# Optimization experiments

Hardware: AMD Instinct MI355X
Metric: run time of the kernel (lower is better)

Reference implementation:

```python
import jax, jax.numpy as jnp
import numpy as np

NUM_HEADS = 8
LN_EPS = 1e-5


def setup_inputs() -> dict:
    key = jax.random.key(0)
    ks = jax.random.split(key, 8)
    B, H, W, C = 2, 64, 64, 256
    return {
        "x": jax.random.normal(ks[0], (B, H, W, C), dtype=jnp.float32),
        "cond": jax.random.normal(ks[1], (B, C), dtype=jnp.float32),
        "t": jax.random.randint(ks[2], (B,), 0, 100, dtype=jnp.int64),
        "emb_table": jax.random.normal(ks[3], (100, C), dtype=jnp.float32) * 0.02,
        "ada_w": jax.random.normal(ks[4], (C, 2 * C), dtype=jnp.float32) * 0.02,
        "ada_b": jnp.zeros((2 * C,), dtype=jnp.float32),
        "qkv_w": jax.random.normal(ks[5], (C, 3 * C), dtype=jnp.float32) * 0.02,
        "qkv_b": jnp.zeros((3 * C,), dtype=jnp.float32),
        "proj_w": jax.random.normal(ks[6], (C, C), dtype=jnp.float32) * 0.02,
        "proj_b": jnp.zeros((C,), dtype=jnp.float32),
    }


def reference(x, cond, t, emb_table, ada_w, ada_b, qkv_w, qkv_b, proj_w, proj_b):
    B, H, W, C = x.shape
    N = H * W
    h = NUM_HEADS
    d = C // h
    scale = d ** -0.5

    x = x.reshape(B, N, C)

    # AdaLayerNorm (adalayernorm_abs): timestep embedding -> SiLU -> Linear -> scale/shift
    emb = emb_table[t]                                # [B, C]
    ss = jax.nn.silu(emb) @ ada_w + ada_b             # [B, 2C]
    sc, sh = jnp.split(ss, 2, axis=-1)                # each [B, C]
    mu = jnp.mean(x, axis=-1, keepdims=True)
    var = jnp.var(x, axis=-1, keepdims=True)
    xn = (x - mu) * jax.lax.rsqrt(var + LN_EPS)       # LN without affine
    x = xn * (1.0 + sc[:, None, :]) + sh[:, None, :]

    # QKV projection and head split
    qkv = (x @ qkv_w + qkv_b).reshape(B, N, 3, h, d)
    qkv = jnp.transpose(qkv, (2, 0, 3, 1, 4))          # [3, B, h, N, d]
    q, k, v = qkv[0], qkv[1], qkv[2]

    # Manual attention: full [B, h, N, N] scores (matches original module)
    attn = jnp.einsum('bhnd,bhmd->bhnm', q, k) * scale
    attn = jax.nn.softmax(attn, axis=-1)
    out = jnp.einsum('bhnm,bhmd->bhnd', attn, v)       # [B, h, N, d]
    out = jnp.transpose(out, (0, 2, 1, 3)).reshape(B, N, C)

    out = (out.reshape(B, H, W, C) @ proj_w) + proj_b
    return out
```

## Files before the change

kernel.cpp:

```cpp
#include <hip/hip_runtime.h>
#include <hip/hip_bf16.h>
#include <stdint.h>

typedef __attribute__((ext_vector_type(8))) short bfrag;
typedef __attribute__((ext_vector_type(4))) short bfrag4;
typedef __attribute__((ext_vector_type(4))) float f32x4;
typedef __attribute__((ext_vector_type(2))) float f32x2;
typedef __attribute__((ext_vector_type(2))) unsigned int u32x2;

__device__ inline short f2bf(float f) {
  union { float f; uint32_t u; } v; v.f = f;
  uint32_t u = v.u;
  uint32_t r = (u + 0x7fffu + ((u >> 16) & 1u)) >> 16;
  return (short)r;
}
__device__ inline float bf2f(short s) {
  return __builtin_bit_cast(float, (uint32_t)((uint32_t)(uint16_t)s << 16));
}

#if __has_builtin(__builtin_amdgcn_cvt_pk_bf16_f32)
typedef __attribute__((ext_vector_type(2))) __bf16 bf16x2_t;
__device__ inline uint32_t pack_bf16(float a, float b) {
  bf16x2_t r = __builtin_amdgcn_cvt_pk_bf16_f32(a, b);
  return __builtin_bit_cast(uint32_t, r);
}
#else
__device__ inline uint32_t pack_bf16(float a, float b) {
  uint32_t ua = __builtin_bit_cast(uint32_t, a) + 0x8000u;
  uint32_t ub = __builtin_bit_cast(uint32_t, b) + 0x8000u;
  return __builtin_amdgcn_perm(ub, ua, 0x07060302);
}
#endif

__global__ __launch_bounds__(256) void prep_kernel(
    const float* __restrict__ emb_table, const int* __restrict__ t,
    const float* __restrict__ ada_w, const float* __restrict__ ada_b,
    float* __restrict__ scsh,
    const float* __restrict__ qkv_w, short* __restrict__ qkv_wt,
    const float* __restrict__ proj_w, short* __restrict__ proj_wt) {
  __shared__ float smem[64 * 65];
  const int blk = blockIdx.x;
  const int tid = threadIdx.x;
  if (blk < 16) {
    float* se = smem;
    float* part = smem + 256;
    int b = blk >> 3, ox = blk & 7;
    int tt = t[b];
    float e = emb_table[tt * 256 + tid];
    se[tid] = e / (1.f + __expf(-e));
    __syncthreads();
    int ol = tid & 63, kc = tid >> 6;
    int o = ox * 64 + ol;
    float acc = 0.f;
#pragma unroll 8
    for (int k = kc * 64; k < (kc + 1) * 64; ++k) acc += se[k] * ada_w[k * 512 + o];
    part[tid] = acc;
    __syncthreads();
    if (tid < 64) {
      int oo = ox * 64 + tid;
      scsh[b * 512 + oo] =
          part[tid] + part[64 + tid] + part[128 + tid] + part[192 + tid] + ada_b[oo];
    }
  } else {
    const float* W; short* Wt; int N, lb;
    if (blk < 64) { W = qkv_w; Wt = qkv_wt; N = 768; lb = blk - 16; }
    else          { W = proj_w; Wt = proj_wt; N = 256; lb = blk - 64; }
    float (*tile)[65] = (float(*)[65])smem;
    int k0 = (lb & 3) * 64, n0 = (lb >> 2) * 64;
    int r = tid >> 2, c0 = (tid & 3) * 16;
    const float* src = W + (long)(k0 + r) * N + n0 + c0;
#pragma unroll
    for (int j = 0; j < 16; j += 4) {
      float4 v = *(const float4*)(src + j);
      tile[r][c0 + j] = v.x; tile[r][c0 + j + 1] = v.y;
      tile[r][c0 + j + 2] = v.z; tile[r][c0 + j + 3] = v.w;
    }
    __syncthreads();
    int nl = tid >> 2, kc = (tid & 3) * 16;
    short outv[16];
#pragma unroll
    for (int j = 0; j < 16; ++j) outv[j] = f2bf(tile[kc + j][nl]);
    short* dst = Wt + (long)(n0 + nl) * 256 + k0 + kc;
    *(bfrag*)dst = *(bfrag*)&outv[0];
    *(bfrag*)(dst + 8) = *(bfrag*)&outv[8];
  }
}

__global__ __launch_bounds__(256) void ln_kernel(const float* __restrict__ x,
                                                 const float* __restrict__ scsh,
                                                 short* __restrict__ xb) {
  int row = blockIdx.x * 4 + (threadIdx.x >> 6);
  int b = row >> 12;
  int lane = threadIdx.x & 63;
  float4 v = *(const float4*)(x + (long)row * 256 + lane * 4);
  float s = v.x + v.y + v.z + v.w;
  float sq = v.x * v.x + v.y * v.y + v.z * v.z + v.w * v.w;
#pragma unroll
  for (int off = 32; off > 0; off >>= 1) {
    s += __shfl_xor(s, off);
    sq += __shfl_xor(sq, off);
  }
  float mu = s * (1.f / 256.f);
  float var = sq * (1.f / 256.f) - mu * mu;
  float rstd = rsqrtf(var + 1e-5f);
  const float* scp = scsh + b * 512 + lane * 4;
  float4 sc = *(const float4*)scp;
  float4 sh = *(const float4*)(scp + 256);
  float y0 = (v.x - mu) * rstd * (1.f + sc.x) + sh.x;
  float y1 = (v.y - mu) * rstd * (1.f + sc.y) + sh.y;
  float y2 = (v.z - mu) * rstd * (1.f + sc.z) + sh.z;
  float y3 = (v.w - mu) * rstd * (1.f + sc.w) + sh.w;
  u32x2 o; o.x = pack_bf16(y0, y1); o.y = pack_bf16(y2, y3);
  *(u32x2*)&xb[(long)row * 256 + lane * 4] = o;
}

__global__ __launch_bounds__(256) void gemm_qkv(const short* __restrict__ A,
                                                const short* __restrict__ Bt,
                                                const float* __restrict__ bias,
                                                float qscale,
                                                short* __restrict__ qk,
                                                short* __restrict__ vT) {
  __shared__ short As[128 * 40];
  __shared__ short Bs[64 * 40];
  const int mt = blockIdx.x, nt = blockIdx.y;
  const int tid = threadIdx.x;
  const int w = tid >> 6, lane = tid & 63, l16 = lane & 15, quad = lane >> 4;
  const int ar = tid >> 1, ak = (tid & 1) * 16;
  const int br = tid >> 2, bk = (tid & 3) * 8;
  f32x4 acc[2][4] = {};
  const short* Arow = A + (long)(mt * 128 + ar) * 256 + ak;
  const short* Brow = Bt + (long)(nt * 64 + br) * 256 + bk;
  bfrag a8a = *(const bfrag*)Arow;
  bfrag a8b = *(const bfrag*)(Arow + 8);
  bfrag b8  = *(const bfrag*)Brow;
  for (int kk = 0; kk < 8; ++kk) {
    __syncthreads();
    *(bfrag*)&As[ar * 40 + ak] = a8a;
    *(bfrag*)&As[ar * 40 + ak + 8] = a8b;
    *(bfrag*)&Bs[br * 40 + bk] = b8;
    __syncthreads();
    int kn = (kk < 7) ? (kk + 1) : 7;
    a8a = *(const bfrag*)(Arow + kn * 32);
    a8b = *(const bfrag*)(Arow + kn * 32 + 8);
    b8  = *(const bfrag*)(Brow + kn * 32);
    bfrag a0 = *(const bfrag*)&As[(w * 32 + l16) * 40 + quad * 8];
    bfrag a1 = *(const bfrag*)&As[(w * 32 + 16 + l16) * 40 + quad * 8];
#pragma unroll
    for (int c = 0; c < 4; ++c) {
      bfrag bf = *(const bfrag*)&Bs[(c * 16 + l16) * 40 + quad * 8];
      acc[0][c] = __builtin_amdgcn_mfma_f32_16x16x32_bf16(a0, bf, acc[0][c], 0, 0, 0);
      acc[1][c] = __builtin_amdgcn_mfma_f32_16x16x32_bf16(a1, bf, acc[1][c], 0, 0, 0);
    }
  }
  const int rowb = mt * 128 + w * 32 + quad * 4;
  if (nt < 8) {
#pragma unroll
    for (int rg = 0; rg < 2; ++rg) {
      int row0 = rowb + rg * 16;
#pragma unroll
      for (int c = 0; c < 4; ++c) {
        int col = nt * 64 + c * 16 + l16;
        float bv = bias[col];
        float mult = (col < 256) ? qscale : 1.0f;
#pragma unroll
        for (int r = 0; r < 4; ++r)
          qk[(long)(row0 + r) * 512 + col] = f2bf((acc[rg][c][r] + bv) * mult);
      }
    }
  } else {
    const int bb = mt >> 5;
#pragma unroll
    for (int rg = 0; rg < 2; ++rg) {
      int keyl = (rowb + rg * 16) & 4095;
#pragma unroll
      for (int c = 0; c < 4; ++c) {
        int col = nt * 64 + c * 16 + l16;
        float bv = bias[col];
        int d = col - 512;
        u32x2 dd;
        dd.x = pack_bf16(acc[rg][c][0] + bv, acc[rg][c][1] + bv);
        dd.y = pack_bf16(acc[rg][c][2] + bv, acc[rg][c][3] + bv);
        *(u32x2*)&vT[((long)(bb * 8 + (d >> 5)) * 32 + (d & 31)) * 4096 + keyl] = dd;
      }
    }
  }
}

__global__ __launch_bounds__(256) void attn_kernel(const short* __restrict__ qk,
                                                   const short* __restrict__ vT,
                                                   short* __restrict__ OpB,
                                                   float* __restrict__ lpart) {
  const int blk = blockIdx.x;
  const int qt = blk & 15;
  const int bh = (blk >> 4) & 15;
  const int ks = blk >> 8;
  const int b = bh >> 3, hh = bh & 7;
  const int tid = threadIdx.x;
  const int w = tid >> 6, lane = tid & 63, l16 = lane & 15, quad = lane >> 4;

  __shared__ short Ks[2][64 * 40];
  __shared__ short Vt[2][32 * 68];

  const long rowbase = (long)b * 4096;
  const int qrow0 = qt * 256 + w * 64 + l16;
  bfrag qf[4];
#pragma unroll
  for (int g = 0; g < 4; ++g)
    qf[g] = *(const bfrag*)&qk[(rowbase + qrow0 + g * 16) * 512 + hh * 32 + quad * 8];

  f32x4 o0[4] = {}, o1[4] = {};
  f32x2 lsum[4] = {};

  const int si = tid >> 2, sk = (tid & 3) * 8;
  const int vrow = tid >> 3, vcol = (tid & 7) * 8;
  const short* ksrc = qk + rowbase * 512 + 256 + hh * 32 + (long)si * 512 + sk;
  const short* vsrc = vT + ((long)bh * 32 + vrow) * 4096 + vcol;

  const int kt0 = ks * 16;
  bfrag k8 = *(const bfrag*)(ksrc + (long)kt0 * 64 * 512);
  bfrag v8 = *(const bfrag*)(vsrc + kt0 * 64);

  int buf = 0;
  for (int i = 0; i < 16; ++i) {
    *(bfrag*)&Ks[buf][si * 40 + sk] = k8;
    *(bfrag*)&Vt[buf][vrow * 68 + vcol] = v8;
    __syncthreads();
    int nn = (i < 15) ? (i + 1) : 15;
    k8 = *(const bfrag*)(ksrc + (long)(kt0 + nn) * 64 * 512);
    v8 = *(const bfrag*)(vsrc + (kt0 + nn) * 64);

#pragma unroll
    for (int nt = 0; nt < 4; ++nt) {
      bfrag kf = *(const bfrag*)&Ks[buf][(nt * 16 + l16) * 40 + quad * 8];
      f32x4 z = {0,0,0,0};
      f32x4 s[4];
      s[0] = __builtin_amdgcn_mfma_f32_16x16x32_bf16(kf, qf[0], z, 0, 0, 0);
      s[1] = __builtin_amdgcn_mfma_f32_16x16x32_bf16(kf, qf[1], z, 0, 0, 0);
      s[2] = __builtin_amdgcn_mfma_f32_16x16x32_bf16(kf, qf[2], z, 0, 0, 0);
      s[3] = __builtin_amdgcn_mfma_f32_16x16x32_bf16(kf, qf[3], z, 0, 0, 0);
      bfrag4 pb[4];
#pragma unroll
      for (int g = 0; g < 4; ++g) {
        float p0 = __builtin_amdgcn_exp2f(s[g][0]);
        float p1 = __builtin_amdgcn_exp2f(s[g][1]);
        float p2 = __builtin_amdgcn_exp2f(s[g][2]);
        float p3 = __builtin_amdgcn_exp2f(s[g][3]);
        f32x2 pa = {p0, p1}, pc = {p2, p3};
        lsum[g] += pa; lsum[g] += pc;
        u32x2 pk; pk.x = pack_bf16(p0, p1); pk.y = pack_bf16(p2, p3);
        pb[g] = __builtin_bit_cast(bfrag4, pk);
      }
      bfrag4 va = *(const bfrag4*)&Vt[buf][l16 * 68 + nt * 16 + quad * 4];
      bfrag4 vb = *(const bfrag4*)&Vt[buf][(16 + l16) * 68 + nt * 16 + quad * 4];
#pragma unroll
      for (int g = 0; g < 4; ++g) {
        o0[g] = __builtin_amdgcn_mfma_f32_16x16x16bf16_1k(va, pb[g], o0[g], 0, 0, 0);
        o1[g] = __builtin_amdgcn_mfma_f32_16x16x16bf16_1k(vb, pb[g], o1[g], 0, 0, 0);
      }
    }
    buf ^= 1;
  }
#pragma unroll
  for (int g = 0; g < 4; ++g) {
    float ls = lsum[g].x + lsum[g].y;
    ls += __shfl_xor(ls, 16); ls += __shfl_xor(ls, 32);
    const long pbase = (((long)ks * 16 + bh) * 4096 + qrow0 + g * 16) * 32;
    u32x2 dA, dB;
    dA.x = pack_bf16(o0[g][0], o0[g][1]); dA.y = pack_bf16(o0[g][2], o0[g][3]);
    dB.x = pack_bf16(o1[g][0], o1[g][1]); dB.y = pack_bf16(o1[g][2], o1[g][3]);
    *(u32x2*)&OpB[pbase + quad * 4] = dA;
    *(u32x2*)&OpB[pbase + 16 + quad * 4] = dB;
    if (quad == 0)
      lpart[((long)ks * 16 + bh) * 4096 + qrow0 + g * 16] = ls;
  }
}

__global__ __launch_bounds__(256) void proj_kernel(const short* __restrict__ OpB,
                                                   const float* __restrict__ lpart,
                                                   const short* __restrict__ Bt,
                                                   const float* __restrict__ bias,
                                                   float* __restrict__ out) {
  __shared__ short As[128 * 40];
  __shared__ short Bs[64 * 40];
  const int mt = blockIdx.x, nt = blockIdx.y;
  const int tid = threadIdx.x;
  const int w = tid >> 6, lane = tid & 63, l16 = lane & 15, quad = lane >> 4;
  const int ar = tid >> 1, ak = (tid & 1) * 16;
  const int br = tid >> 2, bk = (tid & 3) * 8;
  f32x4 acc[2][4] = {};

  const int row = mt * 128 + ar;
  const int q = row & 4095, bq = row >> 12;
  const short* Brow = Bt + (long)(nt * 64 + br) * 256 + bk;

  long lb0 = (long)(bq * 8) * 4096 + q;
  bfrag pa[4][2];
  f32x4 pl;
#pragma unroll
  for (int ks = 0; ks < 4; ++ks) {
    long base = (lb0 + (long)ks * 16 * 4096) * 32 + ak;
    pa[ks][0] = *(const bfrag*)&OpB[base];
    pa[ks][1] = *(const bfrag*)&OpB[base + 8];
    pl[ks] = lpart[lb0 + (long)ks * 16 * 4096];
  }
  bfrag b8 = *(const bfrag*)Brow;

  for (int kk = 0; kk < 8; ++kk) {
    float linv = 1.f / (pl[0] + pl[1] + pl[2] + pl[3]);
    short av[16];
#pragma unroll
    for (int h = 0; h < 2; ++h) {
#pragma unroll
      for (int j = 0; j < 8; j += 2) {
        float v0 = (bf2f(pa[0][h][j]) + bf2f(pa[1][h][j]) +
                    bf2f(pa[2][h][j]) + bf2f(pa[3][h][j])) * linv;
        float v1 = (bf2f(pa[0][h][j+1]) + bf2f(pa[1][h][j+1]) +
                    bf2f(pa[2][h][j+1]) + bf2f(pa[3][h][j+1])) * linv;
        *(uint32_t*)&av[h * 8 + j] = pack_bf16(v0, v1);
      }
    }
    __syncthreads();
    *(bfrag*)&As[ar * 40 + ak] = *(bfrag*)&av[0];
    *(bfrag*)&As[ar * 40 + ak + 8] = *(bfrag*)&av[8];
    *(bfrag*)&Bs[br * 40 + bk] = b8;
    __syncthreads();
    int kn = (kk < 7) ? (kk + 1) : 7;
    long lbn = (long)(bq * 8 + kn) * 4096 + q;
#pragma unroll
    for (int ks = 0; ks < 4; ++ks) {
      long base = (lbn + (long)ks * 16 * 4096) * 32 + ak;
      pa[ks][0] = *(const bfrag*)&OpB[base];
      pa[ks][1] = *(const bfrag*)&OpB[base + 8];
      pl[ks] = lpart[lbn + (long)ks * 16 * 4096];
    }
    b8 = *(const bfrag*)(Brow + kn * 32);

    bfrag a0 = *(const bfrag*)&As[(w * 32 + l16) * 40 + quad * 8];
    bfrag a1 = *(const bfrag*)&As[(w * 32 + 16 + l16) * 40 + quad * 8];
#pragma unroll
    for (int c = 0; c < 4; ++c) {
      bfrag bf = *(const bfrag*)&Bs[(c * 16 + l16) * 40 + quad * 8];
      acc[0][c] = __builtin_amdgcn_mfma_f32_16x16x32_bf16(a0, bf, acc[0][c], 0, 0, 0);
      acc[1][c] = __builtin_amdgcn_mfma_f32_16x16x32_bf16(a1, bf, acc[1][c], 0, 0, 0);
    }
  }
  const int rowb = mt * 128 + w * 32 + quad * 4;
#pragma unroll
  for (int rg = 0; rg < 2; ++rg) {
    int row0 = rowb + rg * 16;
#pragma unroll
    for (int c = 0; c < 4; ++c) {
      int col = nt * 64 + c * 16 + l16;
      float bv = bias[col];
#pragma unroll
      for (int r = 0; r < 4; ++r)
        out[(long)(row0 + r) * 256 + col] = acc[rg][c][r] + bv;
    }
  }
}

extern "C" void kernel_launch(void* const* d_in, const int* in_sizes, int n_in,
                              void* d_out, int out_size, void* d_ws, size_t ws_size,
                              hipStream_t stream) {
  const float* x      = (const float*)d_in[0];
  const int*   t      = (const int*)d_in[2];
  const float* emb    = (const float*)d_in[3];
  const float* ada_w  = (const float*)d_in[4];
  const float* ada_b  = (const float*)d_in[5];
  const float* qkv_w  = (const float*)d_in[6];
  const float* qkv_b  = (const float*)d_in[7];
  const float* proj_w = (const float*)d_in[8];
  const float* proj_b = (const float*)d_in[9];

  char* ws = (char*)d_ws;
  float* scsh     = (float*)(ws);
  short* qkv_wt   = (short*)(ws + 4096);
  short* proj_wt  = (short*)(ws + 397312);
  short* xb       = (short*)(ws + 528384);
  short* qk_out   = (short*)(ws + 4722688);
  short* vT       = (short*)(ws + 13111296);
  short* OpB      = (short*)(ws + 21499904);
  float* lpart    = (float*)(ws + 38277120);

  const float QS = 0.17677669529663687f * 1.4426950408889634f;

  prep_kernel<<<80, 256, 0, stream>>>(emb, t, ada_w, ada_b, scsh,
                                      qkv_w, qkv_wt, proj_w, proj_wt);
  ln_kernel<<<2048, 256, 0, stream>>>(x, scsh, xb);
  gemm_qkv<<<dim3(64, 12), 256, 0, stream>>>(xb, qkv_wt, qkv_b, QS, qk_out, vT);
  attn_kernel<<<1024, 256, 0, stream>>>(qk_out, vT, OpB, lpart);
  proj_kernel<<<dim3(64, 4), 256, 0, stream>>>(OpB, lpart, proj_wt, proj_b,
                                               (float*)d_out);
}
```

Measured before the change: 166.7 us.

## Fuse LayerNorm apply into QKV GEMM A-load and merge row stats into prep

Removes the separate LN kernel. Row mean and rstd are now computed by extra blocks of the prep kernel, and the QKV GEMM reads fp32 x directly, applying normalization, scale and shift before packing to bf16 in its A-tile staging. This removes one launch and the bf16 xb round trip through memory. In exchange, each GEMM block re-reads fp32 x (twice the bytes of bf16) once per N-tile across 12 column tiles, and also re-reads the scale and shift vectors.

Measured after the change: 171.5 us. 1.03x slower.

```diff
diff --git a/kernel.cpp b/kernel.cpp
--- a/kernel.cpp
+++ b/kernel.cpp
@@ -37,7 +37,8 @@
     const float* __restrict__ ada_w, const float* __restrict__ ada_b,
     float* __restrict__ scsh,
     const float* __restrict__ qkv_w, short* __restrict__ qkv_wt,
-    const float* __restrict__ proj_w, short* __restrict__ proj_wt) {
+    const float* __restrict__ proj_w, short* __restrict__ proj_wt,
+    const float* __restrict__ x, float2* __restrict__ rowstats) {
   __shared__ float smem[64 * 65];
   const int blk = blockIdx.x;
   const int tid = threadIdx.x;
@@ -61,7 +62,7 @@
       scsh[b * 512 + oo] =
           part[tid] + part[64 + tid] + part[128 + tid] + part[192 + tid] + ada_b[oo];
     }
-  } else {
+  } else if (blk < 80) {
     const float* W; short* Wt; int N, lb;
     if (blk < 64) { W = qkv_w; Wt = qkv_wt; N = 768; lb = blk - 16; }
     else          { W = proj_w; Wt = proj_wt; N = 256; lb = blk - 64; }
@@ -83,43 +84,30 @@
     short* dst = Wt + (long)(n0 + nl) * 256 + k0 + kc;
     *(bfrag*)dst = *(bfrag*)&outv[0];
     *(bfrag*)(dst + 8) = *(bfrag*)&outv[8];
-  }
-}
-
-__global__ __launch_bounds__(256) void ln_kernel(const float* __restrict__ x,
-                                                 const float* __restrict__ scsh,
-                                                 short* __restrict__ xb) {
-  int row = blockIdx.x * 4 + (threadIdx.x >> 6);
-  int b = row >> 12;
-  int lane = threadIdx.x & 63;
-  float4 v = *(const float4*)(x + (long)row * 256 + lane * 4);
-  float s = v.x + v.y + v.z + v.w;
-  float sq = v.x * v.x + v.y * v.y + v.z * v.z + v.w * v.w;
-#pragma unroll
-  for (int off = 32; off > 0; off >>= 1) {
-    s += __shfl_xor(s, off);
-    sq += __shfl_xor(sq, off);
-  }
-  float mu = s * (1.f / 256.f);
-  float var = sq * (1.f / 256.f) - mu * mu;
-  float rstd = rsqrtf(var + 1e-5f);
-  const float* scp = scsh + b * 512 + lane * 4;
-  float4 sc = *(const float4*)scp;
-  float4 sh = *(const float4*)(scp + 256);
-  float y0 = (v.x - mu) * rstd * (1.f + sc.x) + sh.x;
-  float y1 = (v.y - mu) * rstd * (1.f + sc.y) + sh.y;
-  float y2 = (v.z - mu) * rstd * (1.f + sc.z) + sh.z;
-  float y3 = (v.w - mu) * rstd * (1.f + sc.w) + sh.w;
-  u32x2 o; o.x = pack_bf16(y0, y1); o.y = pack_bf16(y2, y3);
-  *(u32x2*)&xb[(long)row * 256 + lane * 4] = o;
-}
-
-__global__ __launch_bounds__(256) void gemm_qkv(const short* __restrict__ A,
-                                                const short* __restrict__ Bt,
-                                                const float* __restrict__ bias,
-                                                float qscale,
-                                                short* __restrict__ qk,
-                                                short* __restrict__ vT) {
+  } else {
+    int row = (blk - 80) * 4 + (tid >> 6);
+    int lane = tid & 63;
+    float4 v = *(const float4*)(x + (long)row * 256 + lane * 4);
+    float s = v.x + v.y + v.z + v.w;
+    float sq = v.x * v.x + v.y * v.y + v.z * v.z + v.w * v.w;
+#pragma unroll
+    for (int off = 32; off > 0; off >>= 1) {
+      s += __shfl_xor(s, off);
+      sq += __shfl_xor(sq, off);
+    }
+    if (lane == 0) {
+      float mu = s * (1.f / 256.f);
+      float var = sq * (1.f / 256.f) - mu * mu;
+      rowstats[row] = make_float2(mu, rsqrtf(var + 1e-5f));
+    }
+  }
+}
+
+__global__ __launch_bounds__(256) void gemm_qkv(
+    const float* __restrict__ x, const float2* __restrict__ rowstats,
+    const float* __restrict__ scsh, const short* __restrict__ Bt,
+    const float* __restrict__ bias, float qscale,
+    short* __restrict__ qk, short* __restrict__ vT) {
   __shared__ short As[128 * 40];
   __shared__ short Bs[64 * 40];
   const int mt = blockIdx.x, nt = blockIdx.y;
@@ -128,21 +116,47 @@
   const int ar = tid >> 1, ak = (tid & 1) * 16;
   const int br = tid >> 2, bk = (tid & 3) * 8;
   f32x4 acc[2][4] = {};
-  const short* Arow = A + (long)(mt * 128 + ar) * 256 + ak;
+  const int row = mt * 128 + ar;
+  const int bb = row >> 12;
+  float2 st = rowstats[row];
+  const float* xrow = x + (long)row * 256;
+  const float* scb = scsh + bb * 512;
   const short* Brow = Bt + (long)(nt * 64 + br) * 256 + bk;
-  bfrag a8a = *(const bfrag*)Arow;
-  bfrag a8b = *(const bfrag*)(Arow + 8);
-  bfrag b8  = *(const bfrag*)Brow;
+
+  float4 xv[4], scv[4], shv[4];
+#pragma unroll
+  for (int j = 0; j < 4; ++j) {
+    xv[j] = *(const float4*)(xrow + ak + 4 * j);
+    scv[j] = *(const float4*)(scb + ak + 4 * j);
+    shv[j] = *(const float4*)(scb + 256 + ak + 4 * j);
+  }
+  bfrag b8 = *(const bfrag*)Brow;
+
   for (int kk = 0; kk < 8; ++kk) {
-    __syncthreads();
-    *(bfrag*)&As[ar * 40 + ak] = a8a;
-    *(bfrag*)&As[ar * 40 + ak + 8] = a8b;
+    short av[16];
+#pragma unroll
+    for (int j = 0; j < 4; ++j) {
+      float y0 = (xv[j].x - st.x) * st.y * (1.f + scv[j].x) + shv[j].x;
+      float y1 = (xv[j].y - st.x) * st.y * (1.f + scv[j].y) + shv[j].y;
+      float y2 = (xv[j].z - st.x) * st.y * (1.f + scv[j].z) + shv[j].z;
+      float y3 = (xv[j].w - st.x) * st.y * (1.f + scv[j].w) + shv[j].w;
+      *(uint32_t*)&av[4 * j] = pack_bf16(y0, y1);
+      *(uint32_t*)&av[4 * j + 2] = pack_bf16(y2, y3);
+    }
+    __syncthreads();
+    *(bfrag*)&As[ar * 40 + ak] = *(bfrag*)&av[0];
+    *(bfrag*)&As[ar * 40 + ak + 8] = *(bfrag*)&av[8];
     *(bfrag*)&Bs[br * 40 + bk] = b8;
     __syncthreads();
     int kn = (kk < 7) ? (kk + 1) : 7;
-    a8a = *(const bfrag*)(Arow + kn * 32);
-    a8b = *(const bfrag*)(Arow + kn * 32 + 8);
-    b8  = *(const bfrag*)(Brow + kn * 32);
+    int c0 = kn * 32 + ak;
+#pragma unroll
+    for (int j = 0; j < 4; ++j) {
+      xv[j] = *(const float4*)(xrow + c0 + 4 * j);
+      scv[j] = *(const float4*)(scb + c0 + 4 * j);
+      shv[j] = *(const float4*)(scb + 256 + c0 + 4 * j);
+    }
+    b8 = *(const bfrag*)(Brow + kn * 32);
     bfrag a0 = *(const bfrag*)&As[(w * 32 + l16) * 40 + quad * 8];
     bfrag a1 = *(const bfrag*)&As[(w * 32 + 16 + l16) * 40 + quad * 8];
 #pragma unroll
@@ -168,7 +182,7 @@
       }
     }
   } else {
-    const int bb = mt >> 5;
+    const int bb2 = mt >> 5;
 #pragma unroll
     for (int rg = 0; rg < 2; ++rg) {
       int keyl = (rowb + rg * 16) & 4095;
@@ -180,7 +194,7 @@
         u32x2 dd;
         dd.x = pack_bf16(acc[rg][c][0] + bv, acc[rg][c][1] + bv);
         dd.y = pack_bf16(acc[rg][c][2] + bv, acc[rg][c][3] + bv);
-        *(u32x2*)&vT[((long)(bb * 8 + (d >> 5)) * 32 + (d & 31)) * 4096 + keyl] = dd;
+        *(u32x2*)&vT[((long)(bb2 * 8 + (d >> 5)) * 32 + (d & 31)) * 4096 + keyl] = dd;
       }
     }
   }
@@ -373,21 +387,22 @@
   const float* proj_b = (const float*)d_in[9];
 
   char* ws = (char*)d_ws;
-  float* scsh     = (float*)(ws);
-  short* qkv_wt   = (short*)(ws + 4096);
-  short* proj_wt  = (short*)(ws + 397312);
-  short* xb       = (short*)(ws + 528384);
-  short* qk_out   = (short*)(ws + 4722688);
-  short* vT       = (short*)(ws + 13111296);
-  short* OpB      = (short*)(ws + 21499904);
-  float* lpart    = (float*)(ws + 38277120);
+  float* scsh      = (float*)(ws);
+  short* qkv_wt    = (short*)(ws + 4096);
+  short* proj_wt   = (short*)(ws + 397312);
+  float2* rowstats = (float2*)(ws + 528384);
+  short* qk_out    = (short*)(ws + 4722688);
+  short* vT        = (short*)(ws + 13111296);
+  short* OpB       = (short*)(ws + 21499904);
+  float* lpart     = (float*)(ws + 38277120);
 
   const float QS = 0.17677669529663687f * 1.4426950408889634f;
 
-  prep_kernel<<<80, 256, 0, stream>>>(emb, t, ada_w, ada_b, scsh,
-                                      qkv_w, qkv_wt, proj_w, proj_wt);
-  ln_kernel<<<2048, 256, 0, stream>>>(x, scsh, xb);
-  gemm_qkv<<<dim3(64, 12), 256, 0, stream>>>(xb, qkv_wt, qkv_b, QS, qk_out, vT);
+  prep_kernel<<<2128, 256, 0, stream>>>(emb, t, ada_w, ada_b, scsh,
+                                        qkv_w, qkv_wt, proj_w, proj_wt,
+                                        x, rowstats);
+  gemm_qkv<<<dim3(64, 12), 256, 0, stream>>>(x, rowstats, scsh, qkv_wt, qkv_b,
+                                             QS, qk_out, vT);
   attn_kernel<<<1024, 256, 0, stream>>>(qk_out, vT, OpB, lpart);
   proj_kernel<<<dim3(64, 4), 256, 0, stream>>>(OpB, lpart, proj_wt, proj_b,
                                                (float*)d_out);
```

## Fold AdaLN scale/shift into per-batch QKV weights and bias, merge prep with LN

Applied to the files above, without the earlier changes.

The adaptive scale (1+sc) is folded into per-batch bf16 copies of the QKV weight. The shift sh is pushed through the weight into a per-batch bias, and the query softmax scale is also folded in. This lets the LayerNorm pass run without waiting on the scale/shift computation, so the prep and LN work merge into one launch and one kernel launch plus dependency is removed. In exchange, the bias blocks recompute the shift projection redundantly and a serial 256-length dot runs per block. Weight memory doubles, and bf16 rounding now applies after the weights are scaled.

Result: slower. 222.7 us (+33.6%).

```diff
diff --git a/kernel.cpp b/kernel.cpp
--- a/kernel.cpp
+++ b/kernel.cpp
@@ -8,6 +8,8 @@
 typedef __attribute__((ext_vector_type(2))) float f32x2;
 typedef __attribute__((ext_vector_type(2))) unsigned int u32x2;
 
+#define QS 0.25504420211296155f
+
 __device__ inline short f2bf(float f) {
   union { float f; uint32_t u; } v; v.f = f;
   uint32_t u = v.u;
@@ -32,43 +34,61 @@
 }
 #endif
 
-__global__ __launch_bounds__(256) void prep_kernel(
+__global__ __launch_bounds__(256) void prep_ln_kernel(
     const float* __restrict__ emb_table, const int* __restrict__ t,
     const float* __restrict__ ada_w, const float* __restrict__ ada_b,
-    float* __restrict__ scsh,
-    const float* __restrict__ qkv_w, short* __restrict__ qkv_wt,
-    const float* __restrict__ proj_w, short* __restrict__ proj_wt) {
-  __shared__ float smem[64 * 65];
+    const float* __restrict__ qkv_w, const float* __restrict__ qkv_b,
+    const float* __restrict__ proj_w,
+    short* __restrict__ qkv_wt, short* __restrict__ proj_wt,
+    float* __restrict__ biasq,
+    const float* __restrict__ x, short* __restrict__ xb) {
   const int blk = blockIdx.x;
   const int tid = threadIdx.x;
-  if (blk < 16) {
-    float* se = smem;
-    float* part = smem + 256;
-    int b = blk >> 3, ox = blk & 7;
-    int tt = t[b];
-    float e = emb_table[tt * 256 + tid];
-    se[tid] = e / (1.f + __expf(-e));
-    __syncthreads();
-    int ol = tid & 63, kc = tid >> 6;
-    int o = ox * 64 + ol;
-    float acc = 0.f;
-#pragma unroll 8
-    for (int k = kc * 64; k < (kc + 1) * 64; ++k) acc += se[k] * ada_w[k * 512 + o];
-    part[tid] = acc;
-    __syncthreads();
-    if (tid < 64) {
-      int oo = ox * 64 + tid;
-      scsh[b * 512 + oo] =
-          part[tid] + part[64 + tid] + part[128 + tid] + part[192 + tid] + ada_b[oo];
-    }
-  } else {
-    const float* W; short* Wt; int N, lb;
-    if (blk < 64) { W = qkv_w; Wt = qkv_wt; N = 768; lb = blk - 16; }
-    else          { W = proj_w; Wt = proj_wt; N = 256; lb = blk - 64; }
-    float (*tile)[65] = (float(*)[65])smem;
-    int k0 = (lb & 3) * 64, n0 = (lb >> 2) * 64;
+  if (blk >= 70) {
+    int row = (blk - 70) * 4 + (tid >> 6);
+    int lane = tid & 63;
+    float4 v = *(const float4*)(x + (long)row * 256 + lane * 4);
+    float s = v.x + v.y + v.z + v.w;
+    float sq = v.x * v.x + v.y * v.y + v.z * v.z + v.w * v.w;
+#pragma unroll
+    for (int off = 32; off > 0; off >>= 1) {
+      s += __shfl_xor(s, off);
+      sq += __shfl_xor(sq, off);
+    }
+    float mu = s * (1.f / 256.f);
+    float var = sq * (1.f / 256.f) - mu * mu;
+    float rstd = rsqrtf(var + 1e-5f);
+    float y0 = (v.x - mu) * rstd;
+    float y1 = (v.y - mu) * rstd;
+    float y2 = (v.z - mu) * rstd;
+    float y3 = (v.w - mu) * rstd;
+    u32x2 o; o.x = pack_bf16(y0, y1); o.y = pack_bf16(y2, y3);
+    *(u32x2*)&xb[(long)row * 256 + lane * 4] = o;
+    return;
+  }
+  __shared__ float silu2[512];
+  __shared__ float aux[512];
+  __shared__ float tile[64][65];
+  {
+    int t0 = t[0], t1 = t[1];
+    float e0 = emb_table[t0 * 256 + tid];
+    silu2[tid] = e0 / (1.f + __expf(-e0));
+    float e1 = emb_table[t1 * 256 + tid];
+    silu2[256 + tid] = e1 / (1.f + __expf(-e1));
+  }
+  __syncthreads();
+  if (blk < 48) {
+    int k0 = (blk & 3) * 64, n0 = (blk >> 2) * 64;
+    if (tid < 128) {
+      int b = tid >> 6, j = tid & 63;
+      float acc = ada_b[k0 + j];
+      const float* sl = silu2 + b * 256;
+#pragma unroll 4
+      for (int m = 0; m < 256; ++m) acc += sl[m] * ada_w[m * 512 + k0 + j];
+      aux[tid] = acc;
+    }
     int r = tid >> 2, c0 = (tid & 3) * 16;
-    const float* src = W + (long)(k0 + r) * N + n0 + c0;
+    const float* src = qkv_w + (long)(k0 + r) * 768 + n0 + c0;
 #pragma unroll
     for (int j = 0; j < 16; j += 4) {
       float4 v = *(const float4*)(src + j);
@@ -77,59 +97,77 @@
     }
     __syncthreads();
     int nl = tid >> 2, kc = (tid & 3) * 16;
+    float nscale = (n0 + nl < 256) ? QS : 1.0f;
+#pragma unroll
+    for (int b = 0; b < 2; ++b) {
+      short outv[16];
+#pragma unroll
+      for (int j = 0; j < 16; ++j)
+        outv[j] = f2bf(tile[kc + j][nl] * (1.f + aux[b * 64 + kc + j]) * nscale);
+      short* dst = qkv_wt + ((long)b * 768 + n0 + nl) * 256 + k0 + kc;
+      *(bfrag*)dst = *(bfrag*)&outv[0];
+      *(bfrag*)(dst + 8) = *(bfrag*)&outv[8];
+    }
+  } else if (blk < 64) {
+    int lb = blk - 48;
+    int k0 = (lb & 3) * 64, n0 = (lb >> 2) * 64;
+    int r = tid >> 2, c0 = (tid & 3) * 16;
+    const float* src = proj_w + (long)(k0 + r) * 256 + n0 + c0;
+#pragma unroll
+    for (int j = 0; j < 16; j += 4) {
+      float4 v = *(const float4*)(src + j);
+      tile[r][c0 + j] = v.x; tile[r][c0 + j + 1] = v.y;
+      tile[r][c0 + j + 2] = v.z; tile[r][c0 + j + 3] = v.w;
+    }
+    __syncthreads();
+    int nl = tid >> 2, kc = (tid & 3) * 16;
     short outv[16];
 #pragma unroll
     for (int j = 0; j < 16; ++j) outv[j] = f2bf(tile[kc + j][nl]);
-    short* dst = Wt + (long)(n0 + nl) * 256 + k0 + kc;
+    short* dst = proj_wt + (long)(n0 + nl) * 256 + k0 + kc;
     *(bfrag*)dst = *(bfrag*)&outv[0];
     *(bfrag*)(dst + 8) = *(bfrag*)&outv[8];
-  }
-}
-
-__global__ __launch_bounds__(256) void ln_kernel(const float* __restrict__ x,
-                                                 const float* __restrict__ scsh,
-                                                 short* __restrict__ xb) {
-  int row = blockIdx.x * 4 + (threadIdx.x >> 6);
-  int b = row >> 12;
-  int lane = threadIdx.x & 63;
-  float4 v = *(const float4*)(x + (long)row * 256 + lane * 4);
-  float s = v.x + v.y + v.z + v.w;
-  float sq = v.x * v.x + v.y * v.y + v.z * v.z + v.w * v.w;
-#pragma unroll
-  for (int off = 32; off > 0; off >>= 1) {
-    s += __shfl_xor(s, off);
-    sq += __shfl_xor(sq, off);
-  }
-  float mu = s * (1.f / 256.f);
-  float var = sq * (1.f / 256.f) - mu * mu;
-  float rstd = rsqrtf(var + 1e-5f);
-  const float* scp = scsh + b * 512 + lane * 4;
-  float4 sc = *(const float4*)scp;
-  float4 sh = *(const float4*)(scp + 256);
-  float y0 = (v.x - mu) * rstd * (1.f + sc.x) + sh.x;
-  float y1 = (v.y - mu) * rstd * (1.f + sc.y) + sh.y;
-  float y2 = (v.z - mu) * rstd * (1.f + sc.z) + sh.z;
-  float y3 = (v.w - mu) * rstd * (1.f + sc.w) + sh.w;
-  u32x2 o; o.x = pack_bf16(y0, y1); o.y = pack_bf16(y2, y3);
-  *(u32x2*)&xb[(long)row * 256 + lane * 4] = o;
+  } else {
+    {
+      int b = tid >> 7, k = (tid & 127);
+#pragma unroll
+      for (int h = 0; h < 2; ++h) {
+        int kk = k + h * 128;
+        float acc = ada_b[256 + kk];
+        const float* sl = silu2 + b * 256;
+#pragma unroll 4
+        for (int m = 0; m < 256; ++m) acc += sl[m] * ada_w[m * 512 + 256 + kk];
+        aux[b * 256 + kk] = acc;
+      }
+    }
+    __syncthreads();
+    int gi = (blk - 64) * 256 + tid;
+    int b = gi / 768, col = gi % 768;
+    float acc = qkv_b[col];
+    const float* sh = aux + b * 256;
+#pragma unroll 4
+    for (int k = 0; k < 256; ++k) acc += sh[k] * qkv_w[(long)k * 768 + col];
+    if (col < 256) acc *= QS;
+    biasq[b * 768 + col] = acc;
+  }
 }
 
 __global__ __launch_bounds__(256) void gemm_qkv(const short* __restrict__ A,
-                                                const short* __restrict__ Bt,
-                                                const float* __restrict__ bias,
-                                                float qscale,
+                                                const short* __restrict__ Wt,
+                                                const float* __restrict__ biasq,
                                                 short* __restrict__ qk,
                                                 short* __restrict__ vT) {
   __shared__ short As[128 * 40];
   __shared__ short Bs[64 * 40];
   const int mt = blockIdx.x, nt = blockIdx.y;
+  const int bb = mt >> 5;
   const int tid = threadIdx.x;
   const int w = tid >> 6, lane = tid & 63, l16 = lane & 15, quad = lane >> 4;
   const int ar = tid >> 1, ak = (tid & 1) * 16;
   const int br = tid >> 2, bk = (tid & 3) * 8;
   f32x4 acc[2][4] = {};
   const short* Arow = A + (long)(mt * 128 + ar) * 256 + ak;
-  const short* Brow = Bt + (long)(nt * 64 + br) * 256 + bk;
+  const short* Brow = Wt + ((long)bb * 768 + nt * 64 + br) * 256 + bk;
   bfrag a8a = *(const bfrag*)Arow;
   bfrag a8b = *(const bfrag*)(Arow + 8);
   bfrag b8  = *(const bfrag*)Brow;
@@ -160,22 +198,20 @@
 #pragma unroll
       for (int c = 0; c < 4; ++c) {
         int col = nt * 64 + c * 16 + l16;
-        float bv = bias[col];
-        float mult = (col < 256) ? qscale : 1.0f;
+        float bv = biasq[bb * 768 + col];
 #pragma unroll
         for (int r = 0; r < 4; ++r)
-          qk[(long)(row0 + r) * 512 + col] = f2bf((acc[rg][c][r] + bv) * mult);
+          qk[(long)(row0 + r) * 512 + col] = f2bf(acc[rg][c][r] + bv);
       }
     }
   } else {
-    const int bb = mt >> 5;
 #pragma unroll
     for (int rg = 0; rg < 2; ++rg) {
       int keyl = (rowb + rg * 16) & 4095;
 #pragma unroll
       for (int c = 0; c < 4; ++c) {
         int col = nt * 64 + c * 16 + l16;
-        float bv = bias[col];
+        float bv = biasq[bb * 768 + col];
         int d = col - 512;
         u32x2 dd;
         dd.x = pack_bf16(acc[rg][c][0] + bv, acc[rg][c][1] + bv);
@@ -373,21 +409,18 @@
   const float* proj_b = (const float*)d_in[9];
 
   char* ws = (char*)d_ws;
-  float* scsh     = (float*)(ws);
-  short* qkv_wt   = (short*)(ws + 4096);
-  short* proj_wt  = (short*)(ws + 397312);
-  short* xb       = (short*)(ws + 528384);
-  short* qk_out   = (short*)(ws + 4722688);
-  short* vT       = (short*)(ws + 13111296);
-  short* OpB      = (short*)(ws + 21499904);
-  float* lpart    = (float*)(ws + 38277120);
-
-  const float QS = 0.17677669529663687f * 1.4426950408889634f;
-
-  prep_kernel<<<80, 256, 0, stream>>>(emb, t, ada_w, ada_b, scsh,
-                                      qkv_w, qkv_wt, proj_w, proj_wt);
-  ln_kernel<<<2048, 256, 0, stream>>>(x, scsh, xb);
-  gemm_qkv<<<dim3(64, 12), 256, 0, stream>>>(xb, qkv_wt, qkv_b, QS, qk_out, vT);
+  short* qkv_wt   = (short*)(ws);
+  short* proj_wt  = (short*)(ws + 786432);
+  float* biasq    = (float*)(ws + 917504);
+  short* xb       = (short*)(ws + 1048576);
+  short* qk_out   = (short*)(ws + 5242880);
+  short* vT       = (short*)(ws + 13631488);
+  short* OpB      = (short*)(ws + 17825792);
+  float* lpart    = (float*)(ws + 34603008);
+
+  prep_ln_kernel<<<2118, 256, 0, stream>>>(emb, t, ada_w, ada_b, qkv_w, qkv_b,
+                                           proj_w, qkv_wt, proj_wt, biasq, x, xb);
+  gemm_qkv<<<dim3(64, 12), 256, 0, stream>>>(xb, qkv_wt, biasq, qk_out, vT);
   attn_kernel<<<1024, 256, 0, stream>>>(qk_out, vT, OpB, lpart);
   proj_kernel<<<dim3(64, 4), 256, 0, stream>>>(OpB, lpart, proj_wt, proj_b,
                                                (float*)d_out);
```
